# Optimization experiments

Hardware: AMD Instinct MI355X
Metric: run time of the kernel (lower is better)

## Reference

```python
import jax, jax.numpy as jnp
import numpy as np

NEG_SLOPE = 0.2  # PyG GATConv default leaky_relu slope


def _gat_layer(x, W, att_src, att_dst, bias, src, dst, num_nodes, heads, out_c, concat):
    # x: [N, F_in] -> h: [N, H, C]
    h = (x @ W).reshape(num_nodes, heads, out_c)
    a_src = jnp.einsum('nhc,hc->nh', h, att_src)  # [N, H]
    a_dst = jnp.einsum('nhc,hc->nh', h, att_dst)  # [N, H]
    # edge (src -> dst): attention logit per edge/head
    e = jax.nn.leaky_relu(a_src[src] + a_dst[dst], NEG_SLOPE)  # [E, H]
    # softmax over edges sharing the same destination node
    m = jax.ops.segment_max(e, dst, num_segments=num_nodes)  # [N, H]
    m = jnp.where(jnp.isfinite(m), m, 0.0)
    ex = jnp.exp(e - m[dst])
    denom = jax.ops.segment_sum(ex, dst, num_segments=num_nodes)  # [N, H]
    alpha = ex / (denom[dst] + 1e-16)  # [E, H]
    # weighted scatter-add aggregation
    msg = h[src] * alpha[:, :, None]  # [E, H, C]
    out = jax.ops.segment_sum(msg, dst, num_segments=num_nodes)  # [N, H, C]
    if concat:
        out = out.reshape(num_nodes, heads * out_c)
    else:
        out = out.mean(axis=1)
    return out + bias


def _add_self_loops(edge_index, num_nodes):
    loop = jnp.arange(num_nodes, dtype=edge_index.dtype)
    src = jnp.concatenate([edge_index[0], loop])
    dst = jnp.concatenate([edge_index[1], loop])
    return src, dst


def setup_inputs() -> dict:
    key = jax.random.key(0)
    ks = jax.random.split(key, 9)
    N, F_in, E, H, C, OUT = 30000, 256, 300000, 8, 128, 64
    x = jax.random.normal(ks[0], (N, F_in), dtype=jnp.float32)
    edge_index = jax.random.randint(ks[1], (2, E), 0, N, dtype=jnp.int32)
    s1 = 1.0 / np.sqrt(F_in)
    s2 = 1.0 / np.sqrt(H * C)
    return {
        'x': x,
        'edge_index': edge_index,
        'W1': jax.random.normal(ks[2], (F_in, H * C), dtype=jnp.float32) * s1,
        'att_src1': jax.random.normal(ks[3], (H, C), dtype=jnp.float32) * s2,
        'att_dst1': jax.random.normal(ks[4], (H, C), dtype=jnp.float32) * s2,
        'b1': jnp.zeros((H * C,), dtype=jnp.float32),
        'W2': jax.random.normal(ks[5], (H * C, OUT), dtype=jnp.float32) * s2,
        'att_src2': jax.random.normal(ks[6], (1, OUT), dtype=jnp.float32) * 0.125,
        'att_dst2': jax.random.normal(ks[7], (1, OUT), dtype=jnp.float32) * 0.125,
        'b2': jnp.zeros((OUT,), dtype=jnp.float32),
    }


def reference(x, edge_index, W1, att_src1, att_dst1, b1, W2, att_src2, att_dst2, b2):
    N = x.shape[0]
    src, dst = _add_self_loops(edge_index, N)
    # dropout layers are identity in eval mode
    h = _gat_layer(x, W1, att_src1, att_dst1, b1, src, dst, N, 8, 128, True)
    h = jax.nn.elu(h)
    out = _gat_layer(h, W2, att_src2, att_dst2, b2, src, dst, N, 1, 64, False)
    return jax.nn.log_softmax(out, axis=-1)
```

## Files before the change

kernel.cpp:

```cpp
#include <hip/hip_runtime.h>
#include <math.h>

#define N_NODES 30000
#define F_IN 256
#define E_RAW 300000
#define E_TOT (E_RAW + N_NODES)
#define HEADS 8
#define CH 128
#define HC 1024
#define OUTC 64
#define NEG_SLOPE 0.2f
#define CAP 64
#define LOG2E 1.44269504f

typedef __attribute__((ext_vector_type(8))) short bf16x8;
typedef __attribute__((ext_vector_type(4))) float f32x4;
typedef __attribute__((ext_vector_type(2))) float f32x2;

__device__ __forceinline__ float bf2f(unsigned short u) {
    return __uint_as_float(((unsigned)u) << 16);
}
__device__ __forceinline__ unsigned short f2bf(float f) {
    unsigned b = __float_as_uint(f);
    b += 0x7FFFu + ((b >> 16) & 1u);
    return (unsigned short)(b >> 16);
}
__device__ __forceinline__ void edge_sd(const int* __restrict__ ei, int e, int& s, int& d) {
    if (e < E_RAW) { s = ei[e]; d = ei[E_RAW + e]; }
    else           { s = e - E_RAW; d = s; }
}
__device__ __forceinline__ void async_cp16(const void* g, void* l) {
    __builtin_amdgcn_global_load_lds((const __attribute__((address_space(1))) void*)g,
                                     (__attribute__((address_space(3))) void*)l, 16, 0, 0);
}
__device__ __forceinline__ int slotP(int s) {
    return ((s >> 6) << 6) + ((s >> 2) & 15) + ((s & 3) << 4);
}
__device__ __forceinline__ void wave_sync() {
    __builtin_amdgcn_fence(__ATOMIC_ACQ_REL, "wavefront");
    __builtin_amdgcn_wave_barrier();
}
__device__ __forceinline__ f32x2 pk_fma(f32x2 a, f32x2 b, f32x2 c) {
    f32x2 d;
    asm("v_pk_fma_f32 %0, %1, %2, %3" : "=v"(d) : "v"(a), "v"(b), "v"(c));
    return d;
}

#define NB_CVTX (N_NODES * F_IN / 4 / 256)
#define NB_DEG  ((E_TOT + 255) / 256)
#define NB_W1T  ((F_IN * HC + 255) / 256)
#define NB_W2T  ((HC * OUTC + 255) / 256)
#define NB_PREP (NB_CVTX + NB_DEG + NB_W1T + NB_W2T)

__global__ __launch_bounds__(256)
void prep_kernel(const float* __restrict__ x, unsigned short* __restrict__ xb,
                 const float* __restrict__ W1, unsigned short* __restrict__ W1t,
                 const float* __restrict__ W2, unsigned short* __restrict__ W2t,
                 const int* __restrict__ ei, int* __restrict__ deg)
{
    const int b = blockIdx.x, t = threadIdx.x;
    if (b < NB_CVTX) {
        int i = b * 256 + t;
        const float4 v = reinterpret_cast<const float4*>(x)[i];
        ushort4 o;
        o.x = f2bf(v.x); o.y = f2bf(v.y); o.z = f2bf(v.z); o.w = f2bf(v.w);
        reinterpret_cast<ushort4*>(xb)[i] = o;
    } else if (b < NB_CVTX + NB_DEG) {
        int e = (b - NB_CVTX) * 256 + t;
        if (e < E_TOT) {
            int s, d; edge_sd(ei, e, s, d);
            atomicAdd(&deg[d], 1);
        }
    } else if (b < NB_CVTX + NB_DEG + NB_W1T) {
        int i = (b - NB_CVTX - NB_DEG) * 256 + t;
        if (i < F_IN * HC) {
            int k = i >> 10, n = i & (HC - 1);
            W1t[n * F_IN + k] = f2bf(W1[i]);
        }
    } else {
        int i = (b - NB_CVTX - NB_DEG - NB_W1T) * 256 + t;
        if (i < HC * OUTC) {
            int s = i >> 6, n = i & (OUTC - 1);
            W2t[n * HC + s] = f2bf(W2[slotP(s) * OUTC + n]);
        }
    }
}

__global__ __launch_bounds__(256)
void gemm1_mfma(const unsigned short* __restrict__ A,
                const unsigned short* __restrict__ Bt,
                unsigned* __restrict__ Cp,
                const float* __restrict__ att_src, const float* __restrict__ att_dst,
                float* __restrict__ a_src, float* __restrict__ a_dst, int M)
{
    __shared__ unsigned short Al[128 * 64];
    __shared__ unsigned short Bl[128 * 64];
    __shared__ float s_src[128][2];
    __shared__ float s_dst[128][2];
    const int tid  = threadIdx.x;
    const int wave = tid >> 6, lane = tid & 63;
    const int quad = lane >> 4, l16 = lane & 15;
    const int wr = (wave >> 1) * 64, wc = (wave & 1) * 64;
    const int row0 = blockIdx.y * 128;
    const int col0 = blockIdx.x * 128;

    f32x4 acc[4][4];
#pragma unroll
    for (int i = 0; i < 4; i++)
#pragma unroll
        for (int j = 0; j < 4; j++) acc[i][j] = (f32x4){0.f, 0.f, 0.f, 0.f};

    for (int k0 = 0; k0 < F_IN; k0 += 64) {
#pragma unroll
        for (int p = 0; p < 4; p++) {
            int idx = tid + 256 * p;
            int r = idx >> 3, q = idx & 7;
            async_cp16(A + (size_t)(row0 + r) * F_IN + k0 + ((q ^ (r & 7)) * 8),
                       Al + (size_t)(wave * 64 + 256 * p) * 8);
        }
#pragma unroll
        for (int p = 0; p < 4; p++) {
            int idx = tid + 256 * p;
            int r = idx >> 3, q = idx & 7;
            async_cp16(Bt + (size_t)(col0 + r) * F_IN + k0 + ((q ^ (r & 7)) * 8),
                       Bl + (size_t)(wave * 64 + 256 * p) * 8);
        }
        __syncthreads();
#pragma unroll
        for (int kh = 0; kh < 2; kh++) {
            const int cx = (kh * 4 + quad) ^ (l16 & 7);
            bf16x8 af[4], bg[4];
#pragma unroll
            for (int i = 0; i < 4; i++)
                af[i] = *reinterpret_cast<const bf16x8*>(Al + ((wr + i * 16 + l16) * 8 + cx) * 8);
#pragma unroll
            for (int j = 0; j < 4; j++)
                bg[j] = *reinterpret_cast<const bf16x8*>(Bl + ((wc + j * 16 + l16) * 8 + cx) * 8);
#pragma unroll
            for (int i = 0; i < 4; i++)
#pragma unroll
                for (int j = 0; j < 4; j++)
                    acc[i][j] = __builtin_amdgcn_mfma_f32_16x16x32_bf16(af[i], bg[j], acc[i][j], 0, 0, 0);
        }
        __syncthreads();
    }
    const int D = ((col0 + wc) >> 6) * 16 + l16;
#pragma unroll
    for (int i = 0; i < 4; i++) {
#pragma unroll
        for (int r = 0; r < 4; r++) {
            int row = row0 + wr + i * 16 + quad * 4 + r;
            if (row >= M) continue;
            int w8 = __builtin_amdgcn_cvt_pk_fp8_f32(acc[i][0][r], acc[i][1][r], 0, false);
            w8 = __builtin_amdgcn_cvt_pk_fp8_f32(acc[i][2][r], acc[i][3][r], w8, true);
            Cp[(size_t)row * 256 + D] = (unsigned)w8;
        }
    }
    const float* asv = att_src + blockIdx.x * CH;
    const float* adv = att_dst + blockIdx.x * CH;
    float av[4], dv[4];
#pragma unroll
    for (int j = 0; j < 4; j++) {
        av[j] = asv[wc + j * 16 + l16];
        dv[j] = adv[wc + j * 16 + l16];
    }
#pragma unroll
    for (int i = 0; i < 4; i++) {
#pragma unroll
        for (int r = 0; r < 4; r++) {
            float ps = 0.f, pd = 0.f;
#pragma unroll
            for (int j = 0; j < 4; j++) {
                float cc = acc[i][j][r];
                ps += cc * av[j];
                pd += cc * dv[j];
            }
#pragma unroll
            for (int o = 1; o < 16; o <<= 1) {
                ps += __shfl_xor(ps, o);
                pd += __shfl_xor(pd, o);
            }
            if (l16 == 0) {
                int lr = wr + i * 16 + quad * 4 + r;
                s_src[lr][wc >> 6] = ps;
                s_dst[lr][wc >> 6] = pd;
            }
        }
    }
    __syncthreads();
    if (tid < 128) {
        int row = row0 + tid;
        if (row < M) {
            a_src[row * 8 + blockIdx.x] = (s_src[tid][0] + s_src[tid][1]) * LOG2E;
            a_dst[row * 8 + blockIdx.x] = (s_dst[tid][0] + s_dst[tid][1]) * LOG2E;
        }
    }
}

__global__ __launch_bounds__(256)
void gemm2_mfma(const unsigned short* __restrict__ A,
                const unsigned short* __restrict__ Bt,
                unsigned short* __restrict__ C,
                const float* __restrict__ att_src2, const float* __restrict__ att_dst2,
                float* __restrict__ a_src2, float* __restrict__ a_dst2, int M)
{
    __shared__ unsigned short Al[64 * 64];
    __shared__ unsigned short Bl[64 * 64];
    const int tid  = threadIdx.x;
    const int wave = tid >> 6, lane = tid & 63;
    const int quad = lane >> 4, l16 = lane & 15;
    const int wr = wave * 16;
    const int row0 = blockIdx.x * 64;

    f32x4 acc[4];
#pragma unroll
    for (int j = 0; j < 4; j++) acc[j] = (f32x4){0.f, 0.f, 0.f, 0.f};

    for (int k0 = 0; k0 < HC; k0 += 64) {
#pragma unroll
        for (int p = 0; p < 2; p++) {
            int idx = tid + 256 * p;
            int r = idx >> 3, q = idx & 7;
            async_cp16(A + (size_t)(row0 + r) * HC + k0 + ((q ^ (r & 7)) * 8),
                       Al + (size_t)(wave * 64 + 256 * p) * 8);
        }
#pragma unroll
        for (int p = 0; p < 2; p++) {
            int idx = tid + 256 * p;
            int r = idx >> 3, q = idx & 7;
            async_cp16(Bt + (size_t)r * HC + k0 + ((q ^ (r & 7)) * 8),
                       Bl + (size_t)(wave * 64 + 256 * p) * 8);
        }
        __syncthreads();
#pragma unroll
        for (int kh = 0; kh < 2; kh++) {
            const int cx = (kh * 4 + quad) ^ (l16 & 7);
            bf16x8 af, bg[4];
            af = *reinterpret_cast<const bf16x8*>(Al + ((wr + l16) * 8 + cx) * 8);
#pragma unroll
            for (int j = 0; j < 4; j++)
                bg[j] = *reinterpret_cast<const bf16x8*>(Bl + ((j * 16 + l16) * 8 + cx) * 8);
#pragma unroll
            for (int j = 0; j < 4; j++)
                acc[j] = __builtin_amdgcn_mfma_f32_16x16x32_bf16(af, bg[j], acc[j], 0, 0, 0);
        }
        __syncthreads();
    }
    float av[4], dv[4];
#pragma unroll
    for (int j = 0; j < 4; j++) {
        av[j] = att_src2[j * 16 + l16];
        dv[j] = att_dst2[j * 16 + l16];
    }
#pragma unroll
    for (int r = 0; r < 4; r++) {
        int row = row0 + wr + quad * 4 + r;
        float ps = 0.f, pd = 0.f;
#pragma unroll
        for (int j = 0; j < 4; j++) {
            float cc = acc[j][r];
            int col = j * 16 + l16;
            if (row < M) C[(size_t)row * OUTC + col] = f2bf(cc);
            ps += cc * av[j];
            pd += cc * dv[j];
        }
#pragma unroll
        for (int o = 1; o < 16; o <<= 1) {
            ps += __shfl_xor(ps, o);
            pd += __shfl_xor(pd, o);
        }
        if (l16 == 0 && row < M) {
            a_src2[row] = ps;
            a_dst2[row] = pd;
        }
    }
}

__global__ __launch_bounds__(256)
void alloc_kernel(const int* __restrict__ deg, int* __restrict__ rowstart,
                  int* __restrict__ cursor, int* __restrict__ counter)
{
    int d = blockIdx.x * 256 + threadIdx.x;
    int lane = threadIdx.x & 63;
    int v = (d < N_NODES) ? deg[d] : 0;
    int x = v;
#pragma unroll
    for (int o = 1; o < 64; o <<= 1) {
        int y = __shfl_up(x, o);
        if (lane >= o) x += y;
    }
    int excl = x - v;
    int total = __shfl(x, 63);
    int base = 0;
    if (lane == 63) base = atomicAdd(counter, total);
    base = __shfl(base, 63);
    if (d < N_NODES) {
        rowstart[d] = base + excl;
        cursor[d]   = base + excl;
    }
}

__global__ void scatter_kernel(const int* __restrict__ ei, int* __restrict__ cursor,
                               int* __restrict__ csr_src)
{
    int e = blockIdx.x * 256 + threadIdx.x;
    if (e >= E_TOT) return;
    int s, d; edge_sd(ei, e, s, d);
    int pos = atomicAdd(&cursor[d], 1);
    csr_src[pos] = s;
}

struct G4 { int s[4]; };
struct V4 { float a[4]; uint4 u[4]; };

__device__ __forceinline__ G4 g4_load(const int* __restrict__ csr, int start, int c, int degm1) {
    G4 g;
#pragma unroll
    for (int j = 0; j < 4; j++) g.s[j] = csr[start + min(c + j, degm1)];
    return g;
}
__device__ __forceinline__ V4 v4_load(const float* __restrict__ a_src1,
                                      const uint4* __restrict__ h1v,
                                      G4 g, int h, int tl) {
    V4 r;
#pragma unroll
    for (int j = 0; j < 4; j++) {
        r.a[j] = a_src1[g.s[j] * 8 + h];
        r.u[j] = h1v[(size_t)g.s[j] * 64 + tl];
    }
    return r;
}

#define EDGE_PK(al_, uu_, dn_, A_) do { \
    float v_ = fmaxf((al_), NEG_SLOPE * (al_)); \
    float w_ = __builtin_amdgcn_exp2f(v_); \
    (dn_) += w_; \
    f32x2 w2_; w2_.x = w_; w2_.y = w_; \
    (A_)[0] = pk_fma(__builtin_amdgcn_cvt_pk_f32_fp8((int)(uu_).x, false), w2_, (A_)[0]); \
    (A_)[1] = pk_fma(__builtin_amdgcn_cvt_pk_f32_fp8((int)(uu_).x, true ), w2_, (A_)[1]); \
    (A_)[2] = pk_fma(__builtin_amdgcn_cvt_pk_f32_fp8((int)(uu_).y, false), w2_, (A_)[2]); \
    (A_)[3] = pk_fma(__builtin_amdgcn_cvt_pk_f32_fp8((int)(uu_).y, true ), w2_, (A_)[3]); \
    (A_)[4] = pk_fma(__builtin_amdgcn_cvt_pk_f32_fp8((int)(uu_).z, false), w2_, (A_)[4]); \
    (A_)[5] = pk_fma(__builtin_amdgcn_cvt_pk_f32_fp8((int)(uu_).z, true ), w2_, (A_)[5]); \
    (A_)[6] = pk_fma(__builtin_amdgcn_cvt_pk_f32_fp8((int)(uu_).w, false), w2_, (A_)[6]); \
    (A_)[7] = pk_fma(__builtin_amdgcn_cvt_pk_f32_fp8((int)(uu_).w, true ), w2_, (A_)[7]); \
} while (0)

#define CONS4(V_, ad_, dn_, A_) do { \
    EDGE_PK((V_).a[0] + (ad_), (V_).u[0], dn_, A_); \
    EDGE_PK((V_).a[1] + (ad_), (V_).u[1], dn_, A_); \
    EDGE_PK((V_).a[2] + (ad_), (V_).u[2], dn_, A_); \
    EDGE_PK((V_).a[3] + (ad_), (V_).u[3], dn_, A_); \
} while (0)

#define CONS4C(V_, c_, deg_, ad_, dn_, A_) do { \
    float a0_ = ((c_) + 0 < (deg_)) ? (V_).a[0] + (ad_) : -1e30f; EDGE_PK(a0_, (V_).u[0], dn_, A_); \
    float a1_ = ((c_) + 1 < (deg_)) ? (V_).a[1] + (ad_) : -1e30f; EDGE_PK(a1_, (V_).u[1], dn_, A_); \
    float a2_ = ((c_) + 2 < (deg_)) ? (V_).a[2] + (ad_) : -1e30f; EDGE_PK(a2_, (V_).u[2], dn_, A_); \
    float a3_ = ((c_) + 3 < (deg_)) ? (V_).a[3] + (ad_) : -1e30f; EDGE_PK(a3_, (V_).u[3], dn_, A_); \
} while (0)

__device__ __forceinline__ void agg1_epi(int d, int tl, const f32x2* acc, float dn,
                                         const float* __restrict__ b1,
                                         unsigned short* __restrict__ out1)
{
    const float dinv = 1.f / (dn + 1e-16f);
    unsigned short ov[16];
#pragma unroll
    for (int e = 0; e < 16; e++) {
        float v = ((e & 1) ? acc[e >> 1].y : acc[e >> 1].x) * dinv + b1[slotP(16 * tl + e)];
        v = v > 0.f ? v : __expf(v) - 1.f;
        ov[e] = f2bf(v);
    }
    uint4* op = reinterpret_cast<uint4*>(out1 + (size_t)d * HC + 16 * tl);
    op[0] = *reinterpret_cast<uint4*>(&ov[0]);
    op[1] = *reinterpret_cast<uint4*>(&ov[8]);
}

__global__ __launch_bounds__(256)
void agg1_fused(const int* __restrict__ rowstart, const int* __restrict__ degv,
                const int* __restrict__ csr_src,
                const unsigned* __restrict__ h1p,
                const float* __restrict__ a_src1, const float* __restrict__ a_dst1,
                const float* __restrict__ b1, unsigned short* __restrict__ out1)
{
    const int t   = threadIdx.x;
    const int sub = t >> 6;
    const int tl  = t & 63;
    const int h   = tl >> 3;
    const int dA  = blockIdx.x * 8 + sub;
    const int dB  = dA + 4;

    const int startA = __builtin_amdgcn_readfirstlane(rowstart[dA]);
    const int degA   = __builtin_amdgcn_readfirstlane(degv[dA]);
    const int startB = __builtin_amdgcn_readfirstlane(rowstart[dB]);
    const int degB   = __builtin_amdgcn_readfirstlane(degv[dB]);
    const int dmA = degA - 1, dmB = degB - 1;
    const float adA = a_dst1[dA * 8 + h];
    const float adB = a_dst1[dB * 8 + h];
    const uint4* __restrict__ h1v = reinterpret_cast<const uint4*>(h1p);

    float dnA = 0.f, dnB = 0.f;
    f32x2 accA[8], accB[8];
#pragma unroll
    for (int k = 0; k < 8; k++) {
        accA[k] = (f32x2){0.f, 0.f};
        accB[k] = (f32x2){0.f, 0.f};
    }

    G4 sA = g4_load(csr_src, startA, 0, dmA);
    G4 sB = g4_load(csr_src, startB, 0, dmB);
    V4 Ac = v4_load(a_src1, h1v, sA, h, tl);
    V4 Bc = v4_load(a_src1, h1v, sB, h, tl);
    G4 sA1 = g4_load(csr_src, startA, 4, dmA);
    G4 sB1 = g4_load(csr_src, startB, 4, dmB);

#pragma unroll 1
    for (int c = 0; ; c += 4) {
        if (c < degA) {
            const bool more = (c + 4 < degA);
            V4 An;
            if (more) { An = v4_load(a_src1, h1v, sA1, h, tl); sA1 = g4_load(csr_src, startA, c + 8, dmA); }
            if (c + 4 <= degA) { CONS4(Ac, adA, dnA, accA); }
            else               { CONS4C(Ac, c, degA, adA, dnA, accA); }
            if (more) Ac = An;
        }
        if (c < degB) {
            const bool more = (c + 4 < degB);
            V4 Bn;
            if (more) { Bn = v4_load(a_src1, h1v, sB1, h, tl); sB1 = g4_load(csr_src, startB, c + 8, dmB); }
            if (c + 4 <= degB) { CONS4(Bc, adB, dnB, accB); }
            else               { CONS4C(Bc, c, degB, adB, dnB, accB); }
            if (more) Bc = Bn;
        }
        if (c + 4 >= degA && c + 4 >= degB) break;
    }

    agg1_epi(dA, tl, accA, dnA, b1, out1);
    agg1_epi(dB, tl, accB, dnB, b1, out1);
}

__global__ __launch_bounds__(256)
void agg2_lsm(const int* __restrict__ rowstart, const int* __restrict__ degv,
              const int* __restrict__ csr_src,
              const unsigned short* __restrict__ h2,
              const float* __restrict__ a_src2, const float* __restrict__ a_dst2,
              const float* __restrict__ b2, float* __restrict__ out)
{
    const int t = threadIdx.x;
    const int sub  = t >> 6;
    const int lane = t & 63;
    const int eo   = lane >> 4;
    const int cq   = lane & 15;
    const int d = blockIdx.x * 4 + sub;

    __shared__ float exs[4][CAP];
    __shared__ int   ss[4][CAP];

    const int start = rowstart[d];
    const int deg   = degv[d];

    const float adst = a_dst2[d];
    const uint2* __restrict__ h2v = reinterpret_cast<const uint2*>(h2);
    float denom_part = 0.f;
    float ax = 0.f, ay = 0.f, az = 0.f, aw = 0.f;

    for (int c0 = 0; c0 < deg; c0 += CAP) {
        const int cend = min(deg - c0, CAP);
        for (int c = lane; c < cend; c += 64) {
            int s = csr_src[start + c0 + c];
            ss[sub][c] = s;
            float a = a_src2[s] + adst;
            float v = a > 0.f ? a : NEG_SLOPE * a;
            float ex = __expf(v);
            exs[sub][c] = ex;
            denom_part += ex;
        }
        wave_sync();
        {
            int   cc = eo;
            float w0 = (cc < cend) ? exs[sub][cc] : 0.f;
            int   s0 = (cc < cend) ? ss[sub][cc] : ss[sub][0];
            uint2 u0 = h2v[(size_t)s0 * 16 + cq];
            for (int c = 0; c + 4 < cend; c += 4) {
                int cc1 = c + 4 + eo;
                float w1 = (cc1 < cend) ? exs[sub][cc1] : 0.f;
                int   s1 = (cc1 < cend) ? ss[sub][cc1] : ss[sub][0];
                uint2 u1 = h2v[(size_t)s1 * 16 + cq];
                ax += w0 * __uint_as_float(u0.x << 16);
                ay += w0 * __uint_as_float(u0.x & 0xFFFF0000u);
                az += w0 * __uint_as_float(u0.y << 16);
                aw += w0 * __uint_as_float(u0.y & 0xFFFF0000u);
                w0 = w1; s0 = s1; u0 = u1;
            }
            ax += w0 * __uint_as_float(u0.x << 16);
            ay += w0 * __uint_as_float(u0.x & 0xFFFF0000u);
            az += w0 * __uint_as_float(u0.y << 16);
            aw += w0 * __uint_as_float(u0.y & 0xFFFF0000u);
        }
        wave_sync();
    }
    ax += __shfl_xor(ax, 16); ax += __shfl_xor(ax, 32);
    ay += __shfl_xor(ay, 16); ay += __shfl_xor(ay, 32);
    az += __shfl_xor(az, 16); az += __shfl_xor(az, 32);
    aw += __shfl_xor(aw, 16); aw += __shfl_xor(aw, 32);
#pragma unroll
    for (int o = 32; o > 0; o >>= 1) denom_part += __shfl_xor(denom_part, o);
    const float dinv = 1.f / (denom_part + 1e-16f);

    float4 bb = reinterpret_cast<const float4*>(b2)[cq];
    float v0 = ax * dinv + bb.x;
    float v1 = ay * dinv + bb.y;
    float v2 = az * dinv + bb.z;
    float v3 = aw * dinv + bb.w;
    float m = fmaxf(fmaxf(v0, v1), fmaxf(v2, v3));
#pragma unroll
    for (int o = 1; o < 16; o <<= 1) m = fmaxf(m, __shfl_xor(m, o));
    float ex = __expf(v0 - m) + __expf(v1 - m) + __expf(v2 - m) + __expf(v3 - m);
    float ssum = ex;
#pragma unroll
    for (int o = 1; o < 16; o <<= 1) ssum += __shfl_xor(ssum, o);
    if (eo == 0) {
        float lg = __logf(ssum);
        reinterpret_cast<float4*>(out + (size_t)d * OUTC)[cq] =
            make_float4(v0 - m - lg, v1 - m - lg, v2 - m - lg, v3 - m - lg);
    }
}

extern "C" void kernel_launch(void* const* d_in, const int* in_sizes, int n_in,
                              void* d_out, int out_size, void* d_ws, size_t ws_size,
                              hipStream_t stream)
{
    const float* x   = (const float*)d_in[0];
    const int*   ei  = (const int*)d_in[1];
    const float* W1  = (const float*)d_in[2];
    const float* as1 = (const float*)d_in[3];
    const float* ad1 = (const float*)d_in[4];
    const float* b1  = (const float*)d_in[5];
    const float* W2  = (const float*)d_in[6];
    const float* as2 = (const float*)d_in[7];
    const float* ad2 = (const float*)d_in[8];
    const float* b2  = (const float*)d_in[9];

    char* p = (char*)d_ws;
    auto alloc = [&](size_t bytes) { char* r = p; p += (bytes + 255) & ~(size_t)255; return r; };

    char* region0 = (char*)alloc((size_t)N_NODES * HC * 2);
    unsigned* h1p = (unsigned*)region0;

    char* region1 = (char*)alloc((size_t)N_NODES * HC * 2);
    unsigned short* out1 = (unsigned short*)region1;
    unsigned short* xb   = (unsigned short*)region1;
    unsigned short* W1t  = (unsigned short*)(region1 + (size_t)N_NODES * F_IN * 2 + 256);

    unsigned short* W2t = (unsigned short*)alloc((size_t)OUTC * HC * 2);

    float* a_src1   = (float*)alloc((size_t)N_NODES * HEADS * 4);
    float* a_dst1   = (float*)alloc((size_t)N_NODES * HEADS * 4);
    int*   deg      = (int*)alloc((size_t)(N_NODES + 1) * 4);
    int*   counter  = deg + N_NODES;
    int*   rowstart = (int*)alloc((size_t)N_NODES * 4);
    int*   cursor   = (int*)alloc((size_t)N_NODES * 4);
    int*   csr_src  = (int*)alloc((size_t)E_TOT * 4);

    char* q = region0;
    auto alias = [&](size_t bytes) { char* r = q; q += (bytes + 255) & ~(size_t)255; return r; };
    unsigned short* h2 = (unsigned short*)alias((size_t)N_NODES * OUTC * 2);
    float* a_src2  = (float*)alias((size_t)N_NODES * 4);
    float* a_dst2  = (float*)alias((size_t)N_NODES * 4);

    hipMemsetAsync(deg, 0, (size_t)(N_NODES + 1) * 4, stream);

    prep_kernel<<<NB_PREP, 256, 0, stream>>>(x, xb, W1, W1t, W2, W2t, ei, deg);

    alloc_kernel<<<(N_NODES + 255) / 256, 256, 0, stream>>>(deg, rowstart, cursor, counter);
    scatter_kernel<<<(E_TOT + 255) / 256, 256, 0, stream>>>(ei, cursor, csr_src);

    gemm1_mfma<<<dim3(HC / 128, (N_NODES + 127) / 128), 256, 0, stream>>>(
        xb, W1t, h1p, as1, ad1, a_src1, a_dst1, N_NODES);
    agg1_fused<<<N_NODES / 8, 256, 0, stream>>>(rowstart, deg, csr_src, h1p, a_src1, a_dst1, b1, out1);

    gemm2_mfma<<<(N_NODES + 63) / 64, 256, 0, stream>>>(
        out1, W2t, h2, as2, ad2, a_src2, a_dst2, N_NODES);
    agg2_lsm<<<N_NODES / 4, 256, 0, stream>>>(rowstart, deg, csr_src, h2, a_src2, a_dst2, b2, (float*)d_out);
}
```

Before: 266.0 us.

## Process one destination per wave in agg1 and use nontemporal output stores

The layer-1 aggregation kernel now assigns a single destination node to each wavefront instead of interleaving two destinations per wave, and launches twice as many blocks. The aim is to drop the dual-stream control flow and halve the accumulator registers, which should raise occupancy and stop short-degree nodes from idling while their partner node finishes. The cost is that each wave has fewer independent gathers in flight for hiding memory latency. Output writes in agg1 and agg2 also become nontemporal stores to reduce cache pollution, though out1 is read back by the next GEMM.

```diff
diff --git a/kernel.cpp b/kernel.cpp
--- a/kernel.cpp
+++ b/kernel.cpp
@@ -16,6 +16,7 @@
 typedef __attribute__((ext_vector_type(8))) short bf16x8;
 typedef __attribute__((ext_vector_type(4))) float f32x4;
 typedef __attribute__((ext_vector_type(2))) float f32x2;
+typedef __attribute__((ext_vector_type(4))) unsigned u32x4;
 
 __device__ __forceinline__ float bf2f(unsigned short u) {
     return __uint_as_float(((unsigned)u) << 16);
@@ -360,23 +361,6 @@
     float a3_ = ((c_) + 3 < (deg_)) ? (V_).a[3] + (ad_) : -1e30f; EDGE_PK(a3_, (V_).u[3], dn_, A_); \
 } while (0)
 
-__device__ __forceinline__ void agg1_epi(int d, int tl, const f32x2* acc, float dn,
-                                         const float* __restrict__ b1,
-                                         unsigned short* __restrict__ out1)
-{
-    const float dinv = 1.f / (dn + 1e-16f);
-    unsigned short ov[16];
-#pragma unroll
-    for (int e = 0; e < 16; e++) {
-        float v = ((e & 1) ? acc[e >> 1].y : acc[e >> 1].x) * dinv + b1[slotP(16 * tl + e)];
-        v = v > 0.f ? v : __expf(v) - 1.f;
-        ov[e] = f2bf(v);
-    }
-    uint4* op = reinterpret_cast<uint4*>(out1 + (size_t)d * HC + 16 * tl);
-    op[0] = *reinterpret_cast<uint4*>(&ov[0]);
-    op[1] = *reinterpret_cast<uint4*>(&ov[8]);
-}
-
 __global__ __launch_bounds__(256)
 void agg1_fused(const int* __restrict__ rowstart, const int* __restrict__ degv,
                 const int* __restrict__ csr_src,
@@ -388,56 +372,45 @@
     const int sub = t >> 6;
     const int tl  = t & 63;
     const int h   = tl >> 3;
-    const int dA  = blockIdx.x * 8 + sub;
-    const int dB  = dA + 4;
-
-    const int startA = __builtin_amdgcn_readfirstlane(rowstart[dA]);
-    const int degA   = __builtin_amdgcn_readfirstlane(degv[dA]);
-    const int startB = __builtin_amdgcn_readfirstlane(rowstart[dB]);
-    const int degB   = __builtin_amdgcn_readfirstlane(degv[dB]);
-    const int dmA = degA - 1, dmB = degB - 1;
-    const float adA = a_dst1[dA * 8 + h];
-    const float adB = a_dst1[dB * 8 + h];
+    const int d   = blockIdx.x * 4 + sub;
+
+    const int start = __builtin_amdgcn_readfirstlane(rowstart[d]);
+    const int deg   = __builtin_amdgcn_readfirstlane(degv[d]);
+    const int dm    = deg - 1;
+    const float adst = a_dst1[d * 8 + h];
     const uint4* __restrict__ h1v = reinterpret_cast<const uint4*>(h1p);
 
-    float dnA = 0.f, dnB = 0.f;
-    f32x2 accA[8], accB[8];
-#pragma unroll
-    for (int k = 0; k < 8; k++) {
-        accA[k] = (f32x2){0.f, 0.f};
-        accB[k] = (f32x2){0.f, 0.f};
-    }
-
-    G4 sA = g4_load(csr_src, startA, 0, dmA);
-    G4 sB = g4_load(csr_src, startB, 0, dmB);
-    V4 Ac = v4_load(a_src1, h1v, sA, h, tl);
-    V4 Bc = v4_load(a_src1, h1v, sB, h, tl);
-    G4 sA1 = g4_load(csr_src, startA, 4, dmA);
-    G4 sB1 = g4_load(csr_src, startB, 4, dmB);
+    float dn = 0.f;
+    f32x2 acc[8];
+#pragma unroll
+    for (int k = 0; k < 8; k++) acc[k] = (f32x2){0.f, 0.f};
+
+    G4 sC = g4_load(csr_src, start, 0, dm);
+    V4 vC = v4_load(a_src1, h1v, sC, h, tl);
+    G4 sN = g4_load(csr_src, start, 4, dm);
 
 #pragma unroll 1
-    for (int c = 0; ; c += 4) {
-        if (c < degA) {
-            const bool more = (c + 4 < degA);
-            V4 An;
-            if (more) { An = v4_load(a_src1, h1v, sA1, h, tl); sA1 = g4_load(csr_src, startA, c + 8, dmA); }
-            if (c + 4 <= degA) { CONS4(Ac, adA, dnA, accA); }
-            else               { CONS4C(Ac, c, degA, adA, dnA, accA); }
-            if (more) Ac = An;
-        }
-        if (c < degB) {
-            const bool more = (c + 4 < degB);
-            V4 Bn;
-            if (more) { Bn = v4_load(a_src1, h1v, sB1, h, tl); sB1 = g4_load(csr_src, startB, c + 8, dmB); }
-            if (c + 4 <= degB) { CONS4(Bc, adB, dnB, accB); }
-            else               { CONS4C(Bc, c, degB, adB, dnB, accB); }
-            if (more) Bc = Bn;
-        }
-        if (c + 4 >= degA && c + 4 >= degB) break;
-    }
-
-    agg1_epi(dA, tl, accA, dnA, b1, out1);
-    agg1_epi(dB, tl, accB, dnB, b1, out1);
+    for (int c = 0; c < deg; c += 4) {
+        const bool more = (c + 4 < deg);
+        V4 vN;
+        if (more) { vN = v4_load(a_src1, h1v, sN, h, tl); sN = g4_load(csr_src, start, c + 8, dm); }
+        if (c + 4 <= deg) { CONS4(vC, adst, dn, acc); }
+        else              { CONS4C(vC, c, deg, adst, dn, acc); }
+        if (more) vC = vN;
+    }
+
+    const float dinv = 1.f / (dn + 1e-16f);
+
+    unsigned short ov[16];
+#pragma unroll
+    for (int e = 0; e < 16; e++) {
+        float v = ((e & 1) ? acc[e >> 1].y : acc[e >> 1].x) * dinv + b1[slotP(16 * tl + e)];
+        v = v > 0.f ? v : __expf(v) - 1.f;
+        ov[e] = f2bf(v);
+    }
+    u32x4* op = reinterpret_cast<u32x4*>(out1 + (size_t)d * HC + 16 * tl);
+    __builtin_nontemporal_store(*reinterpret_cast<u32x4*>(&ov[0]), op);
+    __builtin_nontemporal_store(*reinterpret_cast<u32x4*>(&ov[8]), op + 1);
 }
 
 __global__ __launch_bounds__(256)
@@ -522,8 +495,10 @@
     for (int o = 1; o < 16; o <<= 1) ssum += __shfl_xor(ssum, o);
     if (eo == 0) {
         float lg = __logf(ssum);
-        reinterpret_cast<float4*>(out + (size_t)d * OUTC)[cq] =
-            make_float4(v0 - m - lg, v1 - m - lg, v2 - m - lg, v3 - m - lg);
+        f32x4 o4;
+        o4.x = v0 - m - lg; o4.y = v1 - m - lg; o4.z = v2 - m - lg; o4.w = v3 - m - lg;
+        __builtin_nontemporal_store(o4,
+            reinterpret_cast<f32x4*>(out + (size_t)d * OUTC) + cq);
     }
 }
 
@@ -578,7 +553,7 @@
 
     gemm1_mfma<<<dim3(HC / 128, (N_NODES + 127) / 128), 256, 0, stream>>>(
         xb, W1t, h1p, as1, ad1, a_src1, a_dst1, N_NODES);
-    agg1_fused<<<N_NODES / 8, 256, 0, stream>>>(rowstart, deg, csr_src, h1p, a_src1, a_dst1, b1, out1);
+    agg1_fused<<<N_NODES / 4, 256, 0, stream>>>(rowstart, deg, csr_src, h1p, a_src1, a_dst1, b1, out1);
 
     gemm2_mfma<<<(N_NODES + 63) / 64, 256, 0, stream>>>(
         out1, W2t, h2, as2, ad2, a_src2, a_dst2, N_NODES);
```

Result: no change. 267.4 us (+0.5%).
